# Kernel optimization log

Hardware: AMD Instinct MI355X
Metric: run time of the kernel (lower is better)

Reference implementation:

```python
import jax, jax.numpy as jnp
import numpy as np

S, B, E = 1024, 64, 1024   # src_seq_len, batch, encoder_hidden_size
H, A = 1024, 1024          # decoder hidden, attention dim
EMB, V = 512, 32000        # embedding_dim, output vocab


def setup_inputs() -> dict:
    key = jax.random.key(0)
    ks = jax.random.split(key, 16)
    sd = lambda n: 1.0 / np.sqrt(n)
    u = lambda k, shape, n: jax.random.uniform(k, shape, jnp.float32, -sd(n), sd(n))
    return {
        "prev_y": jax.random.normal(ks[0], (B, EMB), jnp.float32),
        "prev_h": jax.random.normal(ks[1], (1, B, H), jnp.float32),
        "enc_out": jax.random.normal(ks[2], (S, B, E), jnp.float32),
        # attention params
        "U_w": u(ks[3], (A, E), E), "U_b": u(ks[4], (A,), E),
        "W_w": u(ks[5], (A, H), H), "W_b": u(ks[6], (A,), H),
        "v_w": u(ks[7], (1, A), A), "v_b": u(ks[8], (1,), A),
        # combine + GRU + output params
        "Wc_w": u(ks[9], (H, EMB + E), EMB + E), "Wc_b": u(ks[10], (H,), EMB + E),
        "W_ih": u(ks[11], (3 * H, H), H), "W_hh": u(ks[12], (3 * H, H), H),
        "b_ih": u(ks[13], (3 * H,), H), "b_hh": u(ks[14], (3 * H,), H),
        "Wout_w": u(ks[15], (V, H), H), "Wout_b": jnp.zeros((V,), jnp.float32),
        "mask": 768,
    }


def reference(prev_y, prev_h, enc_out, U_w, U_b, W_w, W_b, v_w, v_b,
              Wc_w, Wc_b, W_ih, W_hh, b_ih, b_hh, Wout_w, Wout_b, mask):
    s, b, e = enc_out.shape
    h = prev_h[0]                                     # [B,H]
    # --- additive (Bahdanau) attention with multiplicative 0/1 prefix mask ---
    uh = jnp.einsum('sbe,ae->sba', enc_out, U_w) + U_b  # [S,B,A]
    wq = h @ W_w.T + W_b                                # [B,A]
    scores = (jnp.tanh(uh + wq) @ v_w[0] + v_b[0]).T    # [B,S]
    m = min(int(mask), s)
    mask_vec = (jnp.arange(s) < m).astype(scores.dtype) # [S]
    scores = scores * mask_vec                          # multiply, NOT -inf (faithful)
    attn = jax.nn.softmax(scores, axis=1)               # [B,S]
    ctx = jnp.einsum('bs,sbe->be', attn, enc_out)       # [B,E]
    # --- combine + single GRU step (PyTorch gate order r,z,n) ---
    x = jnp.concatenate([prev_y, ctx], axis=1) @ Wc_w.T + Wc_b  # [B,H]
    gi = x @ W_ih.T + b_ih                              # [B,3H]
    gh = h @ W_hh.T + b_hh
    Hh = h.shape[1]
    r = jax.nn.sigmoid(gi[:, :Hh] + gh[:, :Hh])
    z = jax.nn.sigmoid(gi[:, Hh:2 * Hh] + gh[:, Hh:2 * Hh])
    n = jnp.tanh(gi[:, 2 * Hh:] + r * gh[:, 2 * Hh:])
    h_new = (1.0 - z) * n + z * h                       # [B,H]
    # --- output projection + log-softmax ---
    logits = h_new @ Wout_w.T + Wout_b                  # [B,V]
    dec_output = jax.nn.log_softmax(logits, axis=1)
    return dec_output, h_new[None], attn
```

## Files before the change

### kernel.cpp

```cpp
#include <hip/hip_runtime.h>

typedef float f32x4 __attribute__((ext_vector_type(4)));
typedef short short8 __attribute__((ext_vector_type(8)));
typedef unsigned int u32;

#define SEQ   1024
#define VOCAB 32000

__device__ __forceinline__ unsigned short f2bf(float f){
  union { float f; unsigned u; } v; v.f = f;
  unsigned r = v.u + 0x7FFFu + ((v.u >> 16) & 1u);
  return (unsigned short)(r >> 16);
}
__device__ __forceinline__ unsigned pk2(float a, float b){
  return (unsigned)f2bf(a) | ((unsigned)f2bf(b) << 16);
}
__device__ __forceinline__ float bf2f(unsigned short h){
  union { unsigned u; float f; } v; v.u = ((unsigned)h) << 16; return v.f;
}
__device__ __forceinline__ float tanh_fast(float x){
  float a = fminf(fmaxf(x, -15.f), 15.f);
  float e = __expf(2.f * a);
  return (e - 1.f) / (e + 1.f);
}
__device__ __forceinline__ float sigm(float x){ return 1.f / (1.f + expf(-x)); }

__device__ __forceinline__ void ld4(float4* dst, const float* p){
  const float4* q = (const float4*)p;
  dst[0]=q[0]; dst[1]=q[1]; dst[2]=q[2]; dst[3]=q[3];
}
__device__ __forceinline__ void cvt_store(char* base, int row, int kb0, const float4* f){
  int xs = (row & 7) << 4;
  uint4 u;
  u.x = pk2(f[0].x, f[0].y); u.y = pk2(f[0].z, f[0].w);
  u.z = pk2(f[1].x, f[1].y); u.w = pk2(f[1].z, f[1].w);
  *(uint4*)(base + row*128 + (kb0 ^ xs)) = u;
  u.x = pk2(f[2].x, f[2].y); u.y = pk2(f[2].z, f[2].w);
  u.z = pk2(f[3].x, f[3].y); u.w = pk2(f[3].z, f[3].w);
  *(uint4*)(base + row*128 + ((kb0 + 16) ^ xs)) = u;
}
__device__ __forceinline__ void gload_lds16(const void* g, void* l){
  __builtin_amdgcn_global_load_lds((const __attribute__((address_space(1))) u32*)g,
                                   (__attribute__((address_space(3))) u32*)l, 16, 0, 0);
}

__global__ __launch_bounds__(256)
void convert_all(const float* __restrict__ uw, const float* __restrict__ enc,
                 unsigned short* __restrict__ uwb, unsigned short* __restrict__ encb)
{
  const int UWC = 131072;
  const int TOT = UWC + 8388608;
  int stride = gridDim.x * 256;
  for (int c = blockIdx.x*256 + threadIdx.x; c < TOT; c += stride){
    const float* src; unsigned short* dst;
    if (c < UWC){ src = uw + (size_t)c*8;        dst = uwb + (size_t)c*8; }
    else        { size_t e = (size_t)(c-UWC)*8;  src = enc + e; dst = encb + e; }
    float4 f0 = ((const float4*)src)[0], f1 = ((const float4*)src)[1];
    uint4 u;
    u.x = pk2(f0.x,f0.y); u.y = pk2(f0.z,f0.w);
    u.z = pk2(f1.x,f1.y); u.w = pk2(f1.z,f1.w);
    *(uint4*)dst = u;
  }
}

__global__ __launch_bounds__(256)
void score_gemm_bf16(const unsigned short* __restrict__ encb,
                     const unsigned short* __restrict__ uwb,
                     const float* __restrict__ Ub, const float* __restrict__ vw,
                     const float* __restrict__ wqm, const int* __restrict__ maskp,
                     float* __restrict__ scores_part)
{
  __shared__ char smem[65536];
  int m = *maskp; m = m < 0 ? 0 : (m > SEQ ? SEQ : m);
  int bI = blockIdx.x;
  int mtile = bI & 511, ntile = bI >> 9;
  if (mtile * 2 >= m) return;
  int t = threadIdx.x, lane = t & 63, wid = t >> 6;
  int wm = wid >> 1, wn = wid & 1;

  int cswz = (((lane & 7) ^ (lane >> 3)) << 4);
  const char* pa = (const char*)encb + ((size_t)(mtile*128 + wid*8 + (lane>>3)))*2048 + cswz;
  const char* pb = (const char*)uwb  + ((size_t)(ntile*128 + wid*8 + (lane>>3)))*2048 + cswz;

  int aAddr[4], bAddr[4], aXor[4], bXor[4];
  #pragma unroll
  for (int i = 0; i < 4; ++i){
    int ra = wm*64 + i*16 + (lane & 15);
    aAddr[i] = ra * 128; aXor[i] = (ra & 7) << 4;
    int rb = wn*64 + i*16 + (lane & 15);
    bAddr[i] = rb * 128; bXor[i] = (rb & 7) << 4;
  }
  int klane = (lane >> 4) << 4;
  int ldsDst = wid * 1024;

  f32x4 acc[4][4] = {};

  {
    char* bA = smem; char* bB = smem + 16384;
    #pragma unroll
    for (int i = 0; i < 4; ++i){
      gload_lds16(pa + (size_t)i*65536, bA + i*4096 + ldsDst);
      gload_lds16(pb + (size_t)i*65536, bB + i*4096 + ldsDst);
    }
  }

  for (int ks = 0; ks < 16; ++ks){
    if (ks < 15){
      char* bA = smem + ((ks+1)&1)*32768; char* bB = bA + 16384;
      #pragma unroll
      for (int i = 0; i < 4; ++i){
        gload_lds16(pa + (size_t)i*65536 + (ks+1)*128, bA + i*4096 + ldsDst);
        gload_lds16(pb + (size_t)i*65536 + (ks+1)*128, bB + i*4096 + ldsDst);
      }
      asm volatile("s_waitcnt vmcnt(8)" ::: "memory");
    } else {
      asm volatile("s_waitcnt vmcnt(0)" ::: "memory");
    }
    __builtin_amdgcn_s_barrier();
    {
      char* bA = smem + (ks&1)*32768; char* bB = bA + 16384;
      #pragma unroll
      for (int kk = 0; kk < 2; ++kk){
        short8 af[4], bv[4];
        int kb = kk * 64 + klane;
        #pragma unroll
        for (int i = 0; i < 4; ++i){
          af[i] = *(const short8*)(bA + aAddr[i] + (kb ^ aXor[i]));
          bv[i] = *(const short8*)(bB + bAddr[i] + (kb ^ bXor[i]));
        }
        #pragma unroll
        for (int mi = 0; mi < 4; ++mi)
          #pragma unroll
          for (int ni = 0; ni < 4; ++ni)
            acc[mi][ni] = __builtin_amdgcn_mfma_f32_16x16x32_bf16(af[mi], bv[ni], acc[mi][ni], 0, 0, 0);
      }
    }
    __builtin_amdgcn_s_barrier();
  }

  int s_idx = mtile * 2 + wm;
  if (s_idx < m){
    float ubv[4], vwv[4];
    #pragma unroll
    for (int ni = 0; ni < 4; ++ni){
      int nt = ntile*128 + wn*64 + ni*16 + (lane & 15);
      ubv[ni] = Ub[nt]; vwv[ni] = vw[nt];
    }
    #pragma unroll
    for (int mi = 0; mi < 4; ++mi){
      #pragma unroll
      for (int j = 0; j < 4; ++j){
        int b = mi*16 + ((lane >> 4) << 2) + j;
        const float* wqrow = wqm + b * 1024;
        float asum = 0.f;
        #pragma unroll
        for (int ni = 0; ni < 4; ++ni){
          int nt = ntile*128 + wn*64 + ni*16 + (lane & 15);
          float uh = acc[mi][ni][j] + ubv[ni] + wqrow[nt];
          asum += tanh_fast(uh) * vwv[ni];
        }
        asum += __shfl_xor(asum, 1, 64);
        asum += __shfl_xor(asum, 2, 64);
        asum += __shfl_xor(asum, 4, 64);
        asum += __shfl_xor(asum, 8, 64);
        if ((lane & 15) == 0)
          scores_part[(ntile*2 + wn)*65536 + b*1024 + s_idx] = asum;
      }
    }
  }
}

__global__ __launch_bounds__(256, 2)
void score_gemm_f32(const float* __restrict__ enc, const float* __restrict__ Uw,
                    const float* __restrict__ Ub, const float* __restrict__ vw,
                    const float* __restrict__ wqm, const int* __restrict__ maskp,
                    float* __restrict__ scores_part)
{
  __shared__ char smem[65536];
  int m = *maskp; m = m < 0 ? 0 : (m > SEQ ? SEQ : m);
  int bI = blockIdx.x;
  int mtile = bI & 511, ntile = bI >> 9;
  if (mtile * 2 >= m) return;
  int row0 = mtile * 128;
  int t = threadIdx.x, lane = t & 63;
  int wid = t >> 6, wm = wid >> 1, wn = wid & 1;
  int srow = t >> 2;
  int sk4 = (t & 3) << 4;
  int kb0 = (t & 3) << 5;

  const float* Ag0 = enc + (size_t)(row0 + srow) * 1024 + sk4;
  const float* Ag1 = Ag0 + 64 * 1024;
  const float* Bg0 = Uw  + (size_t)(ntile * 128 + srow) * 1024 + sk4;
  const float* Bg1 = Bg0 + 64 * 1024;

  float4 fa0[4], fa1[4], fb0[4], fb1[4];
  int aAddr[4], bAddr[4], aXor[4], bXor[4];
  #pragma unroll
  for (int i = 0; i < 4; ++i){
    int ra = wm*64 + i*16 + (lane & 15);
    aAddr[i] = ra * 128; aXor[i] = (ra & 7) << 4;
    int rb = wn*64 + i*16 + (lane & 15);
    bAddr[i] = rb * 128; bXor[i] = (rb & 7) << 4;
  }
  int klane = (lane >> 4) << 4;
  f32x4 acc[4][4] = {};

  ld4(fa0, Ag0); ld4(fa1, Ag1); ld4(fb0, Bg0); ld4(fb1, Bg1);
  {
    char* bA = smem; char* bB = smem + 16384;
    cvt_store(bA, srow,      kb0, fa0);
    cvt_store(bA, srow + 64, kb0, fa1);
    cvt_store(bB, srow,      kb0, fb0);
    cvt_store(bB, srow + 64, kb0, fb1);
  }
  #pragma unroll 2
  for (int ks = 0; ks < 16; ++ks){
    int buf = ks & 1;
    if (ks < 15){
      int ko = (ks + 1) * 64;
      ld4(fa0, Ag0 + ko); ld4(fa1, Ag1 + ko);
      ld4(fb0, Bg0 + ko); ld4(fb1, Bg1 + ko);
    }
    __syncthreads();
    {
      char* bA = smem + buf * 32768;
      char* bB = bA + 16384;
      #pragma unroll
      for (int kk = 0; kk < 2; ++kk){
        short8 af[4], bv[4];
        int kb = kk * 64 + klane;
        #pragma unroll
        for (int i = 0; i < 4; ++i){
          af[i] = *(const short8*)(bA + aAddr[i] + (kb ^ aXor[i]));
          bv[i] = *(const short8*)(bB + bAddr[i] + (kb ^ bXor[i]));
        }
        #pragma unroll
        for (int mi = 0; mi < 4; ++mi)
          #pragma unroll
          for (int ni = 0; ni < 4; ++ni)
            acc[mi][ni] = __builtin_amdgcn_mfma_f32_16x16x32_bf16(af[mi], bv[ni], acc[mi][ni], 0, 0, 0);
      }
    }
    if (ks < 15){
      int nb = buf ^ 1;
      char* bA = smem + nb * 32768; char* bB = bA + 16384;
      cvt_store(bA, srow,      kb0, fa0);
      cvt_store(bA, srow + 64, kb0, fa1);
      cvt_store(bB, srow,      kb0, fb0);
      cvt_store(bB, srow + 64, kb0, fb1);
    }
  }

  int s_idx = mtile * 2 + wm;
  if (s_idx < m){
    float ubv[4], vwv[4];
    #pragma unroll
    for (int ni = 0; ni < 4; ++ni){
      int nt = ntile*128 + wn*64 + ni*16 + (lane & 15);
      ubv[ni] = Ub[nt]; vwv[ni] = vw[nt];
    }
    #pragma unroll
    for (int mi = 0; mi < 4; ++mi){
      #pragma unroll
      for (int j = 0; j < 4; ++j){
        int b = mi*16 + ((lane >> 4) << 2) + j;
        const float* wqrow = wqm + b * 1024;
        float asum = 0.f;
        #pragma unroll
        for (int ni = 0; ni < 4; ++ni){
          int nt = ntile*128 + wn*64 + ni*16 + (lane & 15);
          float uh = acc[mi][ni][j] + ubv[ni] + wqrow[nt];
          asum += tanh_fast(uh) * vwv[ni];
        }
        asum += __shfl_xor(asum, 1, 64);
        asum += __shfl_xor(asum, 2, 64);
        asum += __shfl_xor(asum, 4, 64);
        asum += __shfl_xor(asum, 8, 64);
        if ((lane & 15) == 0)
          scores_part[(ntile*2 + wn)*65536 + b*1024 + s_idx] = asum;
      }
    }
  }
}

__global__ __launch_bounds__(256)
void gemm_m64(const float* __restrict__ A, const float* __restrict__ Bw,
              const float* __restrict__ bias, float* __restrict__ C,
              float* __restrict__ Cpart, int N, int K, int stepsPerZ)
{
  __shared__ unsigned short sA[2][64 * 40];
  __shared__ unsigned short sB[2][128 * 40];
  int t = threadIdx.x, lane = t & 63, wid = t >> 6;
  int ntile = blockIdx.x, z = blockIdx.z;
  int arow = t >> 2, ak = (t & 3) * 8;
  int brow = t >> 1, bk = (t & 1) * 16;
  const float* Ap = A + (size_t)arow * K + ak + (size_t)z * stepsPerZ * 32;
  const float* Bp = Bw + (size_t)(ntile * 128 + brow) * K + bk + (size_t)z * stepsPerZ * 32;
  int klane = (lane >> 4) << 4;
  f32x4 acc[4][2] = {};
  float4 a0, a1, b0, b1, b2, b3;

  {
    const float4* pa = (const float4*)Ap;
    a0 = pa[0]; a1 = pa[1];
    const float4* pb = (const float4*)Bp;
    b0 = pb[0]; b1 = pb[1]; b2 = pb[2]; b3 = pb[3];
    uint4 u;
    u.x = pk2(a0.x,a0.y); u.y = pk2(a0.z,a0.w);
    u.z = pk2(a1.x,a1.y); u.w = pk2(a1.z,a1.w);
    *(uint4*)((char*)sA[0] + arow*80 + ak*2) = u;
    u.x = pk2(b0.x,b0.y); u.y = pk2(b0.z,b0.w);
    u.z = pk2(b1.x,b1.y); u.w = pk2(b1.z,b1.w);
    *(uint4*)((char*)sB[0] + brow*80 + bk*2) = u;
    u.x = pk2(b2.x,b2.y); u.y = pk2(b2.z,b2.w);
    u.z = pk2(b3.x,b3.y); u.w = pk2(b3.z,b3.w);
    *(uint4*)((char*)sB[0] + brow*80 + bk*2 + 16) = u;
  }

  for (int ks = 0; ks < stepsPerZ; ++ks){
    int buf = ks & 1;
    if (ks + 1 < stepsPerZ){
      int kg = (ks + 1) * 32;
      const float4* pa = (const float4*)(Ap + kg);
      a0 = pa[0]; a1 = pa[1];
      const float4* pb = (const float4*)(Bp + kg);
      b0 = pb[0]; b1 = pb[1]; b2 = pb[2]; b3 = pb[3];
    }
    __syncthreads();
    {
      short8 af[4], bv[2];
      #pragma unroll
      for (int mi = 0; mi < 4; ++mi)
        af[mi] = *(const short8*)((char*)sA[buf] + (mi*16 + (lane & 15))*80 + klane);
      #pragma unroll
      for (int ni = 0; ni < 2; ++ni)
        bv[ni] = *(const short8*)((char*)sB[buf] + (wid*32 + ni*16 + (lane & 15))*80 + klane);
      #pragma unroll
      for (int mi = 0; mi < 4; ++mi)
        #pragma unroll
        for (int ni = 0; ni < 2; ++ni)
          acc[mi][ni] = __builtin_amdgcn_mfma_f32_16x16x32_bf16(af[mi], bv[ni], acc[mi][ni], 0, 0, 0);
    }
    if (ks + 1 < stepsPerZ){
      int nb = buf ^ 1;
      uint4 u;
      u.x = pk2(a0.x,a0.y); u.y = pk2(a0.z,a0.w);
      u.z = pk2(a1.x,a1.y); u.w = pk2(a1.z,a1.w);
      *(uint4*)((char*)sA[nb] + arow*80 + ak*2) = u;
      u.x = pk2(b0.x,b0.y); u.y = pk2(b0.z,b0.w);
      u.z = pk2(b1.x,b1.y); u.w = pk2(b1.z,b1.w);
      *(uint4*)((char*)sB[nb] + brow*80 + bk*2) = u;
      u.x = pk2(b2.x,b2.y); u.y = pk2(b2.z,b2.w);
      u.z = pk2(b3.x,b3.y); u.w = pk2(b3.z,b3.w);
      *(uint4*)((char*)sB[nb] + brow*80 + bk*2 + 16) = u;
    }
  }

  bool multi = (gridDim.z > 1);
  #pragma unroll
  for (int ni = 0; ni < 2; ++ni){
    int cg = ntile*128 + wid*32 + ni*16 + (lane & 15);
    float bz = (bias && !multi) ? bias[cg] : 0.f;
    #pragma unroll
    for (int mi = 0; mi < 4; ++mi){
      int r0 = mi*16 + ((lane >> 4) << 2);
      #pragma unroll
      for (int j = 0; j < 4; ++j){
        float val = acc[mi][ni][j] + bz;
        if (multi) Cpart[((size_t)z*64 + r0 + j)*N + cg] = val;
        else       C[(size_t)(r0 + j)*N + cg] = val;
      }
    }
  }
}

__global__ __launch_bounds__(256)
void reduce8_bias(const float* __restrict__ part, const float* __restrict__ bias,
                  float* __restrict__ out, int N)
{
  int idx = blockIdx.x*256 + threadIdx.x;
  int r = idx / (N >> 2), c4 = (idx % (N >> 2)) * 4;
  f32x4 acc = *(const f32x4*)(bias + c4);
  #pragma unroll
  for (int z = 0; z < 8; ++z)
    acc += *(const f32x4*)(part + ((size_t)z*64 + r)*N + c4);
  *(f32x4*)(out + (size_t)r*N + c4) = acc;
}

__global__ __launch_bounds__(256)
void softmax_attn(const float* __restrict__ sp, const float* __restrict__ vb,
                  const int* __restrict__ maskp, float* __restrict__ attn)
{
  __shared__ float sb[4];
  int b = blockIdx.x, t = threadIdx.x, lane = t & 63, wid = t >> 6;
  int m = *maskp; m = m < 0 ? 0 : (m > SEQ ? SEQ : m);
  float vb0 = vb[0];
  float v[4]; float mx = -1e30f;
  #pragma unroll
  for (int k = 0; k < 4; ++k){
    int s = t + k * 256;
    float x = 0.f;
    if (s < m){
      float a = 0.f;
      #pragma unroll
      for (int p = 0; p < 16; ++p) a += sp[p*65536 + b*1024 + s];
      x = a + vb0;
    }
    v[k] = x; mx = fmaxf(mx, x);
  }
  for (int d = 1; d < 64; d <<= 1) mx = fmaxf(mx, __shfl_xor(mx, d, 64));
  if (lane == 0) sb[wid] = mx;
  __syncthreads();
  mx = fmaxf(fmaxf(sb[0], sb[1]), fmaxf(sb[2], sb[3]));
  float sum = 0.f;
  #pragma unroll
  for (int k = 0; k < 4; ++k){ v[k] = expf(v[k] - mx); sum += v[k]; }
  for (int d = 1; d < 64; d <<= 1) sum += __shfl_xor(sum, d, 64);
  __syncthreads();
  if (lane == 0) sb[wid] = sum;
  __syncthreads();
  sum = sb[0] + sb[1] + sb[2] + sb[3];
  #pragma unroll
  for (int k = 0; k < 4; ++k) attn[b*1024 + t + k*256] = v[k] / sum;
}

__global__ __launch_bounds__(256)
void ctx_bf16(const float* __restrict__ attn, const unsigned short* __restrict__ encb,
              float* __restrict__ ctx_part)
{
  int b = blockIdx.x >> 4, ch = blockIdx.x & 15;
  int t = threadIdx.x;
  __shared__ float a_s[64];
  if (t < 64) a_s[t] = attn[b*1024 + ch*64 + t];
  __syncthreads();
  const unsigned short* base = encb + ((size_t)(ch*64)*64 + b)*1024 + t*4;
  f32x4 acc = {};
  for (int s2 = 0; s2 < 64; ++s2){
    ushort4 vv = *(const ushort4*)(base + (size_t)s2*65536);
    float w = a_s[s2];
    acc.x += w * bf2f(vv.x); acc.y += w * bf2f(vv.y);
    acc.z += w * bf2f(vv.z); acc.w += w * bf2f(vv.w);
  }
  *(f32x4*)(ctx_part + (size_t)(b*16 + ch)*1024 + t*4) = acc;
}

__global__ __launch_bounds__(256)
void ctx_f32(const float* __restrict__ attn, const float* __restrict__ enc,
             float* __restrict__ ctx_part)
{
  int b = blockIdx.x >> 4, ch = blockIdx.x & 15;
  int t = threadIdx.x;
  __shared__ float a_s[64];
  if (t < 64) a_s[t] = attn[b*1024 + ch*64 + t];
  __syncthreads();
  const float* ep = enc + (size_t)(ch * 64) * 65536 + b * 1024 + t * 4;
  f32x4 acc = {};
  for (int s2 = 0; s2 < 64; ++s2){
    f32x4 v = *(const f32x4*)(ep + (size_t)s2 * 65536);
    acc += a_s[s2] * v;
  }
  *(f32x4*)(ctx_part + (size_t)(b*16 + ch)*1024 + t*4) = acc;
}

__global__ __launch_bounds__(256)
void build_xcat(const float* __restrict__ part, const float* __restrict__ py,
                float* __restrict__ xcat)
{
  int b = blockIdx.x, t = threadIdx.x;
  f32x4 acc = {};
  #pragma unroll
  for (int c2 = 0; c2 < 16; ++c2)
    acc += *(const f32x4*)(part + (size_t)(b*16 + c2) * 1024 + t * 4);
  *(f32x4*)(xcat + b*1536 + 512 + t*4) = acc;
  if (t < 128)
    *(f32x4*)(xcat + b*1536 + t*4) = *(const f32x4*)(py + b*512 + t*4);
}

__global__ __launch_bounds__(256)
void gru_fused(const float* __restrict__ gip, const float* __restrict__ ghp,
               const float* __restrict__ b_ih, const float* __restrict__ b_hh,
               const float* __restrict__ h, float* __restrict__ hnew)
{
  int idx = blockIdx.x * 256 + threadIdx.x;
  int b = idx >> 10, i = idx & 1023;
  float gr = b_ih[i], gz = b_ih[1024+i], gn = b_ih[2048+i];
  float hr = b_hh[i], hz = b_hh[1024+i], hn = b_hh[2048+i];
  #pragma unroll
  for (int z = 0; z < 8; ++z){
    const float* p = gip + (size_t)z*196608 + b*3072;
    gr += p[i]; gz += p[1024+i]; gn += p[2048+i];
    const float* q = ghp + (size_t)z*196608 + b*3072;
    hr += q[i]; hz += q[1024+i]; hn += q[2048+i];
  }
  float r  = sigm(gr + hr);
  float zz = sigm(gz + hz);
  float n  = tanhf(gn + r * hn);
  hnew[idx] = (1.f - zz) * n + zz * h[idx];
}

__global__ __launch_bounds__(1024)
void logsoftmax_kernel(float* __restrict__ logits)
{
  __shared__ float sb[16];
  int b = blockIdx.x, t = threadIdx.x, lane = t & 63, wid = t >> 6;
  float* row = logits + (size_t)b * VOCAB;
  float v[32]; float mx = -1e30f;
  #pragma unroll
  for (int k = 0; k < 32; ++k){
    int idx = t + k * 1024;
    if (idx < VOCAB){ v[k] = row[idx]; mx = fmaxf(mx, v[k]); }
    else v[k] = -1e30f;
  }
  for (int d = 1; d < 64; d <<= 1) mx = fmaxf(mx, __shfl_xor(mx, d, 64));
  if (lane == 0) sb[wid] = mx;
  __syncthreads();
  float m2 = -1e30f;
  for (int i = 0; i < 16; ++i) m2 = fmaxf(m2, sb[i]);
  mx = m2;
  float sum = 0.f;
  #pragma unroll
  for (int k = 0; k < 32; ++k){
    int idx = t + k * 1024;
    if (idx < VOCAB) sum += expf(v[k] - mx);
  }
  for (int d = 1; d < 64; d <<= 1) sum += __shfl_xor(sum, d, 64);
  __syncthreads();
  if (lane == 0) sb[wid] = sum;
  __syncthreads();
  float s2 = 0.f;
  for (int i = 0; i < 16; ++i) s2 += sb[i];
  float lse = mx + logf(s2);
  #pragma unroll
  for (int k = 0; k < 32; ++k){
    int idx = t + k * 1024;
    if (idx < VOCAB) row[idx] = v[k] - lse;
  }
}

extern "C" void kernel_launch(void* const* d_in, const int* in_sizes, int n_in,
                              void* d_out, int out_size, void* d_ws, size_t ws_size,
                              hipStream_t stream)
{
  const float* prev_y = (const float*)d_in[0];
  const float* prev_h = (const float*)d_in[1];
  const float* enc    = (const float*)d_in[2];
  const float* U_w    = (const float*)d_in[3];
  const float* U_b    = (const float*)d_in[4];
  const float* W_w    = (const float*)d_in[5];
  const float* W_b    = (const float*)d_in[6];
  const float* v_w    = (const float*)d_in[7];
  const float* v_b    = (const float*)d_in[8];
  const float* Wc_w   = (const float*)d_in[9];
  const float* Wc_b   = (const float*)d_in[10];
  const float* W_ih   = (const float*)d_in[11];
  const float* W_hh   = (const float*)d_in[12];
  const float* b_ih   = (const float*)d_in[13];
  const float* b_hh   = (const float*)d_in[14];
  const float* Wout_w = (const float*)d_in[15];
  const float* Wout_b = (const float*)d_in[16];
  const int*   maskp  = (const int*)d_in[17];

  char* wsb = (char*)d_ws;
  const size_t ENC_B = 134217728ULL;
  const size_t UW_B  = 2097152ULL;
  const size_t FLOATS_B = 26083328ULL;
  bool big = ws_size >= ENC_B + UW_B + FLOATS_B;

  unsigned short* encb = (unsigned short*)wsb;
  unsigned short* uwb  = (unsigned short*)(wsb + ENC_B);
  float* f = (float*)(wsb + (big ? (ENC_B + UW_B) : 0));
  float* scores_part = f;
  float* wq_part     = scores_part + 1048576;
  float* wq          = wq_part + 524288;
  float* ctx_part    = wq + 65536;
  float* xcat        = ctx_part + 1048576;
  float* xvec_part   = xcat + 98304;
  float* xvec        = xvec_part + 524288;
  float* gi_part     = xvec + 65536;
  float* gh_part     = gi_part + 1572864;

  float* out_logp = (float*)d_out;
  float* out_h    = out_logp + 64 * VOCAB;
  float* out_attn = out_h + 65536;

  if (big)
    convert_all<<<2048, 256, 0, stream>>>(U_w, enc, uwb, encb);

  gemm_m64<<<dim3(8,1,8), 256, 0, stream>>>(prev_h, W_w, nullptr, nullptr, wq_part, 1024, 1024, 4);
  reduce8_bias<<<64, 256, 0, stream>>>(wq_part, W_b, wq, 1024);

  if (big)
    score_gemm_bf16<<<4096, 256, 0, stream>>>(encb, uwb, U_b, v_w, wq, maskp, scores_part);
  else
    score_gemm_f32<<<4096, 256, 0, stream>>>(enc, U_w, U_b, v_w, wq, maskp, scores_part);

  softmax_attn<<<64, 256, 0, stream>>>(scores_part, v_b, maskp, out_attn);

  if (big) ctx_bf16<<<1024, 256, 0, stream>>>(out_attn, encb, ctx_part);
  else     ctx_f32<<<1024, 256, 0, stream>>>(out_attn, enc, ctx_part);
  build_xcat<<<64, 256, 0, stream>>>(ctx_part, prev_y, xcat);

  gemm_m64<<<dim3(8,1,8), 256, 0, stream>>>(xcat, Wc_w, nullptr, nullptr, xvec_part, 1024, 1536, 6);
  reduce8_bias<<<64, 256, 0, stream>>>(xvec_part, Wc_b, xvec, 1024);

  gemm_m64<<<dim3(24,1,8), 256, 0, stream>>>(xvec, W_ih, nullptr, nullptr, gi_part, 3072, 1024, 4);
  gemm_m64<<<dim3(24,1,8), 256, 0, stream>>>(prev_h, W_hh, nullptr, nullptr, gh_part, 3072, 1024, 4);
  gru_fused<<<256, 256, 0, stream>>>(gi_part, gh_part, b_ih, b_hh, prev_h, out_h);

  gemm_m64<<<dim3(250,1,1), 256, 0, stream>>>(out_h, Wout_w, Wout_b, out_logp, nullptr, VOCAB, 1024, 32);
  logsoftmax_kernel<<<64, 1024, 0, stream>>>(out_logp);
}
```

Baseline: 763.6 us.

## Halve score GEMM K-tile for higher occupancy and split-K the output projection

The bf16 score GEMM now stages 64-wide K slices (32 steps) instead of 128-wide ones, which halves LDS use to 32KB. It adds a launch-bounds occupancy hint of 4 blocks and a matching swizzle pattern, aiming to hide latency through more resident waves. Separately, the vocab projection is split across 4 K-chunks to fill more CUs, and the partial sums plus bias are reduced inside a fused log-softmax kernel. This costs extra partial-buffer traffic and needs a larger workspace, with a fallback to the old path when the workspace is too small.

```diff
diff --git a/kernel.cpp b/kernel.cpp
--- a/kernel.cpp
+++ b/kernel.cpp
@@ -63,14 +63,14 @@
   }
 }
 
-__global__ __launch_bounds__(256)
+__global__ __launch_bounds__(256, 4)
 void score_gemm_bf16(const unsigned short* __restrict__ encb,
                      const unsigned short* __restrict__ uwb,
                      const float* __restrict__ Ub, const float* __restrict__ vw,
                      const float* __restrict__ wqm, const int* __restrict__ maskp,
                      float* __restrict__ scores_part)
 {
-  __shared__ char smem[65536];
+  __shared__ char smem[32768];
   int m = *maskp; m = m < 0 ? 0 : (m > SEQ ? SEQ : m);
   int bI = blockIdx.x;
   int mtile = bI & 511, ntile = bI >> 9;
@@ -78,62 +78,62 @@
   int t = threadIdx.x, lane = t & 63, wid = t >> 6;
   int wm = wid >> 1, wn = wid & 1;
 
-  int cswz = (((lane & 7) ^ (lane >> 3)) << 4);
-  const char* pa = (const char*)encb + ((size_t)(mtile*128 + wid*8 + (lane>>3)))*2048 + cswz;
-  const char* pb = (const char*)uwb  + ((size_t)(ntile*128 + wid*8 + (lane>>3)))*2048 + cswz;
-
-  int aAddr[4], bAddr[4], aXor[4], bXor[4];
+  int rbase = wid*32 + (lane >> 2);
+  int scol  = (((lane & 3) ^ ((lane >> 3) & 3)) << 4);
+  const char* pa = (const char*)encb + (size_t)(mtile*128 + rbase)*2048 + scol;
+  const char* pb = (const char*)uwb  + (size_t)(ntile*128 + rbase)*2048 + scol;
+
+  int kb = (lane >> 4) << 4;
+  int aOff[4], bOff[4];
   #pragma unroll
   for (int i = 0; i < 4; ++i){
     int ra = wm*64 + i*16 + (lane & 15);
-    aAddr[i] = ra * 128; aXor[i] = (ra & 7) << 4;
+    aOff[i] = ra*64 + (kb ^ (((ra >> 1) & 3) << 4));
     int rb = wn*64 + i*16 + (lane & 15);
-    bAddr[i] = rb * 128; bXor[i] = (rb & 7) << 4;
-  }
-  int klane = (lane >> 4) << 4;
-  int ldsDst = wid * 1024;
+    bOff[i] = rb*64 + (kb ^ (((rb >> 1) & 3) << 4));
+  }
+  int ldsW = wid * 2048;
 
   f32x4 acc[4][4] = {};
 
   {
-    char* bA = smem; char* bB = smem + 16384;
-    #pragma unroll
-    for (int i = 0; i < 4; ++i){
-      gload_lds16(pa + (size_t)i*65536, bA + i*4096 + ldsDst);
-      gload_lds16(pb + (size_t)i*65536, bB + i*4096 + ldsDst);
-    }
-  }
-
-  for (int ks = 0; ks < 16; ++ks){
-    if (ks < 15){
-      char* bA = smem + ((ks+1)&1)*32768; char* bB = bA + 16384;
-      #pragma unroll
-      for (int i = 0; i < 4; ++i){
-        gload_lds16(pa + (size_t)i*65536 + (ks+1)*128, bA + i*4096 + ldsDst);
-        gload_lds16(pb + (size_t)i*65536 + (ks+1)*128, bB + i*4096 + ldsDst);
-      }
-      asm volatile("s_waitcnt vmcnt(8)" ::: "memory");
+    char* dA = smem + ldsW;
+    char* dB = smem + 8192 + ldsW;
+    gload_lds16(pa,         dA);
+    gload_lds16(pa + 32768, dA + 1024);
+    gload_lds16(pb,         dB);
+    gload_lds16(pb + 32768, dB + 1024);
+  }
+
+  for (int ks = 0; ks < 32; ++ks){
+    if (ks < 31){
+      char* base = smem + ((ks+1)&1)*16384;
+      char* dA = base + ldsW;
+      char* dB = base + 8192 + ldsW;
+      int ko = (ks+1)*64;
+      gload_lds16(pa + ko,         dA);
+      gload_lds16(pa + 32768 + ko, dA + 1024);
+      gload_lds16(pb + ko,         dB);
+      gload_lds16(pb + 32768 + ko, dB + 1024);
+      asm volatile("s_waitcnt vmcnt(4)" ::: "memory");
     } else {
       asm volatile("s_waitcnt vmcnt(0)" ::: "memory");
     }
     __builtin_amdgcn_s_barrier();
     {
-      char* bA = smem + (ks&1)*32768; char* bB = bA + 16384;
-      #pragma unroll
-      for (int kk = 0; kk < 2; ++kk){
-        short8 af[4], bv[4];
-        int kb = kk * 64 + klane;
+      char* bufA = smem + (ks&1)*16384;
+      char* bufB = bufA + 8192;
+      short8 af[4], bv[4];
+      #pragma unroll
+      for (int i = 0; i < 4; ++i){
+        af[i] = *(const short8*)(bufA + aOff[i]);
+        bv[i] = *(const short8*)(bufB + bOff[i]);
+      }
+      #pragma unroll
+      for (int mi = 0; mi < 4; ++mi)
         #pragma unroll
-        for (int i = 0; i < 4; ++i){
-          af[i] = *(const short8*)(bA + aAddr[i] + (kb ^ aXor[i]));
-          bv[i] = *(const short8*)(bB + bAddr[i] + (kb ^ bXor[i]));
-        }
-        #pragma unroll
-        for (int mi = 0; mi < 4; ++mi)
-          #pragma unroll
-          for (int ni = 0; ni < 4; ++ni)
-            acc[mi][ni] = __builtin_amdgcn_mfma_f32_16x16x32_bf16(af[mi], bv[ni], acc[mi][ni], 0, 0, 0);
-      }
+        for (int ni = 0; ni < 4; ++ni)
+          acc[mi][ni] = __builtin_amdgcn_mfma_f32_16x16x32_bf16(af[mi], bv[ni], acc[mi][ni], 0, 0, 0);
     }
     __builtin_amdgcn_s_barrier();
   }
@@ -496,6 +496,50 @@
   float zz = sigm(gz + hz);
   float n  = tanhf(gn + r * hn);
   hnew[idx] = (1.f - zz) * n + zz * h[idx];
+}
+
+__global__ __launch_bounds__(1024)
+void logsoftmax_fused4(const float* __restrict__ part, const float* __restrict__ bias,
+                       float* __restrict__ out)
+{
+  __shared__ float sb[16];
+  int b = blockIdx.x, t = threadIdx.x, lane = t & 63, wid = t >> 6;
+  float v[32]; float mx = -1e30f;
+  #pragma unroll
+  for (int k = 0; k < 32; ++k){
+    int idx = t + k * 1024;
+    if (idx < VOCAB){
+      float x = bias[idx];
+      #pragma unroll
+      for (int z = 0; z < 4; ++z) x += part[((size_t)(z*64 + b))*VOCAB + idx];
+      v[k] = x; mx = fmaxf(mx, x);
+    } else v[k] = -1e30f;
+  }
+  for (int d = 1; d < 64; d <<= 1) mx = fmaxf(mx, __shfl_xor(mx, d, 64));
+  if (lane == 0) sb[wid] = mx;
+  __syncthreads();
+  float m2 = -1e30f;
+  for (int i = 0; i < 16; ++i) m2 = fmaxf(m2, sb[i]);
+  mx = m2;
+  float sum = 0.f;
+  #pragma unroll
+  for (int k = 0; k < 32; ++k){
+    int idx = t + k * 1024;
+    if (idx < VOCAB) sum += expf(v[k] - mx);
+  }
+  for (int d = 1; d < 64; d <<= 1) sum += __shfl_xor(sum, d, 64);
+  __syncthreads();
+  if (lane == 0) sb[wid] = sum;
+  __syncthreads();
+  float s2 = 0.f;
+  for (int i = 0; i < 16; ++i) s2 += sb[i];
+  float lse = mx + logf(s2);
+  float* row = out + (size_t)b * VOCAB;
+  #pragma unroll
+  for (int k = 0; k < 32; ++k){
+    int idx = t + k * 1024;
+    if (idx < VOCAB) row[idx] = v[k] - lse;
+  }
 }
 
 __global__ __launch_bounds__(1024)
@@ -561,10 +605,12 @@
   const int*   maskp  = (const int*)d_in[17];
 
   char* wsb = (char*)d_ws;
-  const size_t ENC_B = 134217728ULL;
-  const size_t UW_B  = 2097152ULL;
-  const size_t FLOATS_B = 26083328ULL;
-  bool big = ws_size >= ENC_B + UW_B + FLOATS_B;
+  const size_t ENC_B    = 134217728ULL;
+  const size_t UW_B     = 2097152ULL;
+  const size_t FLOATS1_B = 26083328ULL;
+  const size_t FLOATS2_B = FLOATS1_B + 32768000ULL;
+  bool big  = ws_size >= ENC_B + UW_B + FLOATS1_B;
+  bool big2 = ws_size >= ENC_B + UW_B + FLOATS2_B;
 
   unsigned short* encb = (unsigned short*)wsb;
   unsigned short* uwb  = (unsigned short*)(wsb + ENC_B);
@@ -578,6 +624,7 @@
   float* xvec        = xvec_part + 524288;
   float* gi_part     = xvec + 65536;
   float* gh_part     = gi_part + 1572864;
+  float* wout_part   = gh_part + 1572864;
 
   float* out_logp = (float*)d_out;
   float* out_h    = out_logp + 64 * VOCAB;
@@ -607,6 +654,11 @@
   gemm_m64<<<dim3(24,1,8), 256, 0, stream>>>(prev_h, W_hh, nullptr, nullptr, gh_part, 3072, 1024, 4);
   gru_fused<<<256, 256, 0, stream>>>(gi_part, gh_part, b_ih, b_hh, prev_h, out_h);
 
-  gemm_m64<<<dim3(250,1,1), 256, 0, stream>>>(out_h, Wout_w, Wout_b, out_logp, nullptr, VOCAB, 1024, 32);
-  logsoftmax_kernel<<<64, 1024, 0, stream>>>(out_logp);
-}
+  if (big2){
+    gemm_m64<<<dim3(250,1,4), 256, 0, stream>>>(out_h, Wout_w, nullptr, nullptr, wout_part, VOCAB, 1024, 8);
+    logsoftmax_fused4<<<64, 1024, 0, stream>>>(wout_part, Wout_b, out_logp);
+  } else {
+    gemm_m64<<<dim3(250,1,1), 256, 0, stream>>>(out_h, Wout_w, Wout_b, out_logp, nullptr, VOCAB, 1024, 32);
+    logsoftmax_kernel<<<64, 1024, 0, stream>>>(out_logp);
+  }
+}
```

After: 743.1 us. 1.03x faster.
